# Performance work log

Hardware: AMD Instinct MI355X
Metric: run time of the kernel (lower is better)

Reference implementation:

```python
import jax, jax.numpy as jnp
import numpy as np

WS = 8          # window_size
H = 4           # num_heads
C = 128         # embed_dim
D = C // H      # head_dim
L = WS * WS     # tokens per window
B = 4096        # batch * num_windows


def _make_rel_index(ws):
    coords = np.stack(np.meshgrid(np.arange(ws), np.arange(ws), indexing='ij'))  # [2,ws,ws]
    flat = coords.reshape(2, -1)                       # [2, L]
    rel = flat[:, :, None] - flat[:, None, :]          # [2, L, L]
    rel = rel.transpose(1, 2, 0) + ws - 1              # [L, L, 2]
    return (rel[..., 0] * (2 * ws - 1) + rel[..., 1]).astype(np.int32)  # [L, L]


def setup_inputs() -> dict:
    key = jax.random.key(0)
    ks = jax.random.split(key, 10)
    s = 0.02
    return {
        'query': jax.random.normal(ks[0], (B, L, C), jnp.float32),
        'Wq': jax.random.normal(ks[1], (C, C), jnp.float32) * s,
        'bq': jnp.zeros((C,), jnp.float32),
        'Wk': jax.random.normal(ks[2], (C, C), jnp.float32) * s,
        'bk': jnp.zeros((C,), jnp.float32),
        'Wv': jax.random.normal(ks[3], (C, C), jnp.float32) * s,
        'bv': jnp.zeros((C,), jnp.float32),
        'Wo': jax.random.normal(ks[4], (C, C), jnp.float32) * s,
        'bo': jnp.zeros((C,), jnp.float32),
        'bias_table': jax.random.normal(ks[5], ((2 * WS - 1) ** 2, H), jnp.float32) * s,
        'rel_index': jnp.asarray(_make_rel_index(WS)),
    }


def reference(query, Wq, bq, Wk, bk, Wv, bv, Wo, bo, bias_table, rel_index):
    scale = D ** -0.5
    # projections (torch Linear: x @ W.T + b)
    q = (query @ Wq.T + bq).reshape(B, L, H, D).transpose(0, 2, 1, 3)  # [B,H,L,D]
    k = (query @ Wk.T + bk).reshape(B, L, H, D).transpose(0, 2, 1, 3)
    v = (query @ Wv.T + bv).reshape(B, L, H, D).transpose(0, 2, 1, 3)
    attn = jnp.einsum('bhqd,bhkd->bhqk', q, k) * scale               # [B,H,L,L]
    bias = bias_table[rel_index]                                      # [L,L,H]
    attn = attn + bias.transpose(2, 0, 1)[None]                       # add RPB
    attn = jax.nn.softmax(attn, axis=-1)
    out = jnp.einsum('bhqk,bhkd->bqhd', attn, v).reshape(B, L, C)
    out = out @ Wo.T + bo
    return out
```

## Files before the change

### kernel.cpp

```cpp
#include <hip/hip_runtime.h>
#include <hip/hip_bf16.h>

typedef unsigned int u32;
typedef unsigned short u16;
typedef __attribute__((ext_vector_type(8))) short short8;
typedef __attribute__((ext_vector_type(4))) float f32x4;
typedef __attribute__((ext_vector_type(2))) u32 u32x2;

#define LOG2E 1.4426950408889634f
#define SCALE 0.17677669529663687f

__device__ __forceinline__ u16 f2bf(float f) {
    return __builtin_bit_cast(u16, __float2bfloat16(f));
}
__device__ __forceinline__ u32 pkbf(float a, float b) {
    return (u32)f2bf(a) | ((u32)f2bf(b) << 16);
}

__device__ __forceinline__ int sw128(int r, int e) { return r * 128 + (e ^ ((r & 7) << 3)); }
__device__ __forceinline__ int sw64 (int r, int e) { return r * 64  + (e ^ ((r & 7) << 3)); }

__global__ __launch_bounds__(256) void prep_kernel(
    const float* __restrict__ Wq, const float* __restrict__ Wk,
    const float* __restrict__ Wv, const float* __restrict__ Wo,
    const float* __restrict__ bias_table, const int* __restrict__ rel_index,
    u16* __restrict__ wsW, float* __restrict__ wsB)
{
    int idx = blockIdx.x * 256 + threadIdx.x;
    if (idx < 16384) {
        wsW[idx]         = f2bf(Wq[idx] * (SCALE * LOG2E));
        wsW[16384 + idx] = f2bf(Wk[idx]);
        wsW[32768 + idx] = f2bf(Wv[idx]);
        wsW[49152 + idx] = f2bf(Wo[idx]);
        int h = idx >> 12, t = (idx >> 8) & 15, l = (idx >> 2) & 63, r = idx & 3;
        int mt = t >> 2, nt = t & 3, g = l >> 4, c = l & 15;
        int kk = 16 * mt + 4 * g + r, q = 16 * nt + c;
        wsB[idx] = bias_table[rel_index[q * 64 + kk] * 4 + h] * LOG2E;
    }
}

__global__ __launch_bounds__(256, 3) void wattn_kernel(
    const float* __restrict__ x,
    const float* __restrict__ bq, const float* __restrict__ bk,
    const float* __restrict__ bv, const float* __restrict__ bo,
    const u16* __restrict__ Wbf, const float* __restrict__ biasT,
    float* __restrict__ out)
{
    __shared__ u16 smem[24576];

    const int b    = blockIdx.x;
    const int tid  = threadIdx.x;
    const int wid  = tid >> 6;
    const int lane = tid & 63;
    const int g    = lane >> 4;
    const int c    = lane & 15;

    u16* qk = smem + wid * 6144;
    u16* vT = qk + 4096;

    {
        const float* xb = x + (size_t)b * 8192;
        #pragma unroll
        for (int it = 0; it < 8; ++it) {
            int idx = it * 1024 + tid * 4;
            float4 v = *(const float4*)(xb + idx);
            int row = idx >> 7, col = idx & 127;
            u32x2 wv;
            wv.x = pkbf(v.x, v.y);
            wv.y = pkbf(v.z, v.w);
            *(u32x2*)&smem[sw128(row, col)] = wv;
        }
    }
    __syncthreads();

    short8 xa[4][4];
    #pragma unroll
    for (int mt = 0; mt < 4; ++mt)
        #pragma unroll
        for (int kt = 0; kt < 4; ++kt)
            xa[mt][kt] = *(const short8*)&smem[sw128(16 * mt + c, 32 * kt + 8 * g)];
    __syncthreads();

    const int h = wid, d0 = 32 * h;
    #pragma unroll
    for (int p = 0; p < 3; ++p) {
        const float* bp = (p == 0) ? bq : (p == 1) ? bk : bv;
        #pragma unroll
        for (int j = 0; j < 2; ++j) {
            int nt = 2 * h + j;
            float bcol = bp[16 * nt + c];
            if (p == 0) bcol *= (SCALE * LOG2E);
            f32x4 acc[4];
            #pragma unroll
            for (int mt = 0; mt < 4; ++mt) { f32x4 t = {bcol, bcol, bcol, bcol}; acc[mt] = t; }
            const u16* W = Wbf + p * 16384 + (16 * nt + c) * 128;
            #pragma unroll
            for (int kt = 0; kt < 4; ++kt) {
                short8 bfr = *(const short8*)(W + 32 * kt + 8 * g);
                #pragma unroll
                for (int mt = 0; mt < 4; ++mt)
                    acc[mt] = __builtin_amdgcn_mfma_f32_16x16x32_bf16(xa[mt][kt], bfr, acc[mt], 0, 0, 0);
            }
            if (p < 2) {
                int colb = p * 32 + 16 * j + c;
                #pragma unroll
                for (int mt = 0; mt < 4; ++mt)
                    #pragma unroll
                    for (int r = 0; r < 4; ++r)
                        qk[sw64(16 * mt + 4 * g + r, colb)] = f2bf(acc[mt][r]);
            } else {
                #pragma unroll
                for (int mt = 0; mt < 4; ++mt) {
                    u32x2 wv;
                    wv.x = pkbf(acc[mt][0], acc[mt][1]);
                    wv.y = pkbf(acc[mt][2], acc[mt][3]);
                    *(u32x2*)&vT[sw64(16 * j + c, 16 * mt + 4 * g)] = wv;
                }
            }
        }
    }

    short8 ka[4], qb[4];
    #pragma unroll
    for (int t = 0; t < 4; ++t) {
        qb[t] = *(const short8*)&qk[sw64(16 * t + c, 8 * g)];
        ka[t] = *(const short8*)&qk[sw64(16 * t + c, 32 + 8 * g)];
    }
    f32x4 accP[4][4];
    const f32x4* bT = (const f32x4*)(biasT + h * 4096);
    #pragma unroll
    for (int mt = 0; mt < 4; ++mt)
        #pragma unroll
        for (int nt = 0; nt < 4; ++nt)
            accP[mt][nt] = __builtin_amdgcn_mfma_f32_16x16x32_bf16(
                ka[mt], qb[nt], bT[(mt * 4 + nt) * 64 + lane], 0, 0, 0);

    float rinv[4];
    #pragma unroll
    for (int nt = 0; nt < 4; ++nt) {
        float m = accP[0][nt][0];
        #pragma unroll
        for (int mt = 0; mt < 4; ++mt)
            #pragma unroll
            for (int r = 0; r < 4; ++r) m = fmaxf(m, accP[mt][nt][r]);
        m = fmaxf(m, __shfl_xor(m, 16, 64));
        m = fmaxf(m, __shfl_xor(m, 32, 64));
        float s = 0.f;
        #pragma unroll
        for (int mt = 0; mt < 4; ++mt)
            #pragma unroll
            for (int r = 0; r < 4; ++r) {
                float e = exp2f(accP[mt][nt][r] - m);
                accP[mt][nt][r] = e;
                s += e;
            }
        s += __shfl_xor(s, 16, 64);
        s += __shfl_xor(s, 32, 64);
        rinv[nt] = 1.0f / s;
    }

    #pragma unroll
    for (int mt = 0; mt < 4; ++mt)
        #pragma unroll
        for (int nt = 0; nt < 4; ++nt) {
            u32x2 wv;
            wv.x = pkbf(accP[mt][nt][0], accP[mt][nt][1]);
            wv.y = pkbf(accP[mt][nt][2], accP[mt][nt][3]);
            *(u32x2*)&qk[sw64(16 * nt + c, 16 * mt + 4 * g)] = wv;
        }

    f32x4 accO[2][4];
    #pragma unroll
    for (int mD = 0; mD < 2; ++mD)
        #pragma unroll
        for (int nt = 0; nt < 4; ++nt) { f32x4 z = {0.f, 0.f, 0.f, 0.f}; accO[mD][nt] = z; }
    #pragma unroll
    for (int kt = 0; kt < 2; ++kt) {
        short8 va[2];
        #pragma unroll
        for (int mD = 0; mD < 2; ++mD)
            va[mD] = *(const short8*)&vT[sw64(16 * mD + c, 32 * kt + 8 * g)];
        #pragma unroll
        for (int nt = 0; nt < 4; ++nt) {
            short8 pb = *(const short8*)&qk[sw64(16 * nt + c, 32 * kt + 8 * g)];
            #pragma unroll
            for (int mD = 0; mD < 2; ++mD)
                accO[mD][nt] = __builtin_amdgcn_mfma_f32_16x16x32_bf16(va[mD], pb, accO[mD][nt], 0, 0, 0);
        }
    }
    __syncthreads();

    #pragma unroll
    for (int mD = 0; mD < 2; ++mD)
        #pragma unroll
        for (int nt = 0; nt < 4; ++nt) {
            float riv = rinv[nt];
            u32x2 wv;
            wv.x = pkbf(accO[mD][nt][0] * riv, accO[mD][nt][1] * riv);
            wv.y = pkbf(accO[mD][nt][2] * riv, accO[mD][nt][3] * riv);
            *(u32x2*)&smem[sw128(16 * nt + c, d0 + 16 * mD + 4 * g)] = wv;
        }
    __syncthreads();

    short8 ha[4][4];
    #pragma unroll
    for (int mt = 0; mt < 4; ++mt)
        #pragma unroll
        for (int kt = 0; kt < 4; ++kt)
            ha[mt][kt] = *(const short8*)&smem[sw128(16 * mt + c, 32 * kt + 8 * g)];
    const u16* Wo_ = Wbf + 3 * 16384;
    float* ob = out + (size_t)b * 8192;
    #pragma unroll
    for (int j = 0; j < 2; ++j) {
        int nt = 2 * wid + j;
        float bocol = bo[16 * nt + c];
        f32x4 acc[4];
        #pragma unroll
        for (int mt = 0; mt < 4; ++mt) { f32x4 t = {bocol, bocol, bocol, bocol}; acc[mt] = t; }
        const u16* W = Wo_ + (16 * nt + c) * 128;
        #pragma unroll
        for (int kt = 0; kt < 4; ++kt) {
            short8 wf = *(const short8*)(W + 32 * kt + 8 * g);
            #pragma unroll
            for (int mt = 0; mt < 4; ++mt)
                acc[mt] = __builtin_amdgcn_mfma_f32_16x16x32_bf16(ha[mt][kt], wf, acc[mt], 0, 0, 0);
        }
        #pragma unroll
        for (int mt = 0; mt < 4; ++mt)
            #pragma unroll
            for (int r = 0; r < 4; ++r)
                ob[(16 * mt + 4 * g + r) * 128 + 16 * nt + c] = acc[mt][r];
    }
}

extern "C" void kernel_launch(void* const* d_in, const int* in_sizes, int n_in,
                              void* d_out, int out_size, void* d_ws, size_t ws_size,
                              hipStream_t stream)
{
    const float* query      = (const float*)d_in[0];
    const float* Wq         = (const float*)d_in[1];
    const float* bq         = (const float*)d_in[2];
    const float* Wk         = (const float*)d_in[3];
    const float* bk         = (const float*)d_in[4];
    const float* Wv         = (const float*)d_in[5];
    const float* bv         = (const float*)d_in[6];
    const float* Wo         = (const float*)d_in[7];
    const float* bo         = (const float*)d_in[8];
    const float* bias_table = (const float*)d_in[9];
    const int*   rel_index  = (const int*)d_in[10];

    u16*   wsW = (u16*)d_ws;
    float* wsB = (float*)((char*)d_ws + 131072);

    prep_kernel<<<dim3(64), dim3(256), 0, stream>>>(Wq, Wk, Wv, Wo, bias_table, rel_index, wsW, wsB);
    wattn_kernel<<<dim3(4096), dim3(256), 0, stream>>>(query, bq, bk, bv, bo, wsW, wsB, (float*)d_out);
}
```

Measured before the change: 127.7 us.

## Keep Q/K/P in registers via transposed MFMA layouts and raise occupancy

The Q and K projections are computed in transposed orientation (W as the A operand) so their accumulator fragments can be packed directly into 16x16x16 bf16 MFMA operands for QK^T. This removes the per-wave LDS staging for Q, K and the softmax probabilities, which also feeds P·V from registers. Shared memory shrinks from 48KB to 32KB, launch bounds rise to 4 blocks per CU, and the output projection is transposed so each lane writes a float4. The risks are extra register pressure from holding packed fragments under a tighter occupancy target, and the smaller K=16 MFMA instructions.

```diff
diff --git a/kernel.cpp b/kernel.cpp
--- a/kernel.cpp
+++ b/kernel.cpp
@@ -3,7 +3,8 @@
 
 typedef unsigned int u32;
 typedef unsigned short u16;
-typedef __attribute__((ext_vector_type(8))) short short8;
+typedef __attribute__((ext_vector_type(8))) short bf16x8;
+typedef __attribute__((ext_vector_type(4))) short bf16x4;
 typedef __attribute__((ext_vector_type(4))) float f32x4;
 typedef __attribute__((ext_vector_type(2))) u32 u32x2;
 
@@ -16,6 +17,21 @@
 __device__ __forceinline__ u32 pkbf(float a, float b) {
     return (u32)f2bf(a) | ((u32)f2bf(b) << 16);
 }
+__device__ __forceinline__ bf16x4 pk4(f32x4 v) {
+    u32x2 p; p.x = pkbf(v[0], v[1]); p.y = pkbf(v[2], v[3]);
+    return __builtin_bit_cast(bf16x4, p);
+}
+
+#if __has_builtin(__builtin_amdgcn_mfma_f32_16x16x16bf16_1k)
+#define MFMA16(A, B, C) __builtin_amdgcn_mfma_f32_16x16x16bf16_1k((A), (B), (C), 0, 0, 0)
+#else
+__device__ __forceinline__ f32x4 mfma16_fb(bf16x4 a, bf16x4 b, f32x4 c) {
+    bf16x8 a8 = {a[0], a[1], a[2], a[3], 0, 0, 0, 0};
+    bf16x8 b8 = {b[0], b[1], b[2], b[3], 0, 0, 0, 0};
+    return __builtin_amdgcn_mfma_f32_16x16x32_bf16(a8, b8, c, 0, 0, 0);
+}
+#define MFMA16(A, B, C) mfma16_fb((A), (B), (C))
+#endif
 
 __device__ __forceinline__ int sw128(int r, int e) { return r * 128 + (e ^ ((r & 7) << 3)); }
 __device__ __forceinline__ int sw64 (int r, int e) { return r * 64  + (e ^ ((r & 7) << 3)); }
@@ -39,14 +55,47 @@
     }
 }
 
-__global__ __launch_bounds__(256, 3) void wattn_kernel(
+__device__ __forceinline__ void proj_qk(
+    const u16* __restrict__ Xs, const u16* __restrict__ W,
+    const float* __restrict__ bp, float bscale,
+    int h, int g, int c, bf16x4 opk[4][2])
+{
+    f32x4 acc[2][4];
+    #pragma unroll
+    for (int CT = 0; CT < 2; ++CT) {
+        float4 bb = *(const float4*)&bp[32 * h + 16 * CT + 4 * g];
+        f32x4 bi = {bb.x * bscale, bb.y * bscale, bb.z * bscale, bb.w * bscale};
+        #pragma unroll
+        for (int nt = 0; nt < 4; ++nt) acc[CT][nt] = bi;
+    }
+    #pragma unroll
+    for (int kt = 0; kt < 4; ++kt) {
+        bf16x8 xs[4];
+        #pragma unroll
+        for (int nt = 0; nt < 4; ++nt)
+            xs[nt] = *(const bf16x8*)&Xs[sw128(16 * nt + c, 32 * kt + 8 * g)];
+        #pragma unroll
+        for (int CT = 0; CT < 2; ++CT) {
+            bf16x8 wf = *(const bf16x8*)(W + (32 * h + 16 * CT + c) * 128 + 32 * kt + 8 * g);
+            #pragma unroll
+            for (int nt = 0; nt < 4; ++nt)
+                acc[CT][nt] = __builtin_amdgcn_mfma_f32_16x16x32_bf16(wf, xs[nt], acc[CT][nt], 0, 0, 0);
+        }
+    }
+    #pragma unroll
+    for (int nt = 0; nt < 4; ++nt)
+        #pragma unroll
+        for (int CT = 0; CT < 2; ++CT) opk[nt][CT] = pk4(acc[CT][nt]);
+}
+
+__global__ __launch_bounds__(256, 4) void wattn_kernel(
     const float* __restrict__ x,
     const float* __restrict__ bq, const float* __restrict__ bk,
     const float* __restrict__ bv, const float* __restrict__ bo,
     const u16* __restrict__ Wbf, const float* __restrict__ biasT,
     float* __restrict__ out)
 {
-    __shared__ u16 smem[24576];
+    __shared__ u16 smem[16384];
 
     const int b    = blockIdx.x;
     const int tid  = threadIdx.x;
@@ -54,9 +103,10 @@
     const int lane = tid & 63;
     const int g    = lane >> 4;
     const int c    = lane & 15;
-
-    u16* qk = smem + wid * 6144;
-    u16* vT = qk + 4096;
+    const int h    = wid;
+
+    u16* Xs = smem;
+    u16* vT = smem + 8192 + wid * 2048;
 
     {
         const float* xb = x + (size_t)b * 8192;
@@ -68,81 +118,74 @@
             u32x2 wv;
             wv.x = pkbf(v.x, v.y);
             wv.y = pkbf(v.z, v.w);
-            *(u32x2*)&smem[sw128(row, col)] = wv;
+            *(u32x2*)&Xs[sw128(row, col)] = wv;
         }
     }
     __syncthreads();
 
-    short8 xa[4][4];
-    #pragma unroll
-    for (int mt = 0; mt < 4; ++mt)
-        #pragma unroll
-        for (int kt = 0; kt < 4; ++kt)
-            xa[mt][kt] = *(const short8*)&smem[sw128(16 * mt + c, 32 * kt + 8 * g)];
-    __syncthreads();
-
-    const int h = wid, d0 = 32 * h;
-    #pragma unroll
-    for (int p = 0; p < 3; ++p) {
-        const float* bp = (p == 0) ? bq : (p == 1) ? bk : bv;
+    bf16x4 qpk[4][2], kpk[4][2];
+    proj_qk(Xs, Wbf,         bq, SCALE * LOG2E, h, g, c, qpk);
+    proj_qk(Xs, Wbf + 16384, bk, 1.0f,          h, g, c, kpk);
+
+    {
+        const u16* Wv_ = Wbf + 32768;
+        f32x4 acc[2][4];
         #pragma unroll
         for (int j = 0; j < 2; ++j) {
-            int nt = 2 * h + j;
-            float bcol = bp[16 * nt + c];
-            if (p == 0) bcol *= (SCALE * LOG2E);
-            f32x4 acc[4];
-            #pragma unroll
-            for (int mt = 0; mt < 4; ++mt) { f32x4 t = {bcol, bcol, bcol, bcol}; acc[mt] = t; }
-            const u16* W = Wbf + p * 16384 + (16 * nt + c) * 128;
-            #pragma unroll
-            for (int kt = 0; kt < 4; ++kt) {
-                short8 bfr = *(const short8*)(W + 32 * kt + 8 * g);
+            float bcol = bv[32 * h + 16 * j + c];
+            #pragma unroll
+            for (int mt = 0; mt < 4; ++mt) { f32x4 t = {bcol, bcol, bcol, bcol}; acc[j][mt] = t; }
+        }
+        #pragma unroll
+        for (int kt = 0; kt < 4; ++kt) {
+            bf16x8 xs[4];
+            #pragma unroll
+            for (int mt = 0; mt < 4; ++mt)
+                xs[mt] = *(const bf16x8*)&Xs[sw128(16 * mt + c, 32 * kt + 8 * g)];
+            #pragma unroll
+            for (int j = 0; j < 2; ++j) {
+                bf16x8 wf = *(const bf16x8*)(Wv_ + (32 * h + 16 * j + c) * 128 + 32 * kt + 8 * g);
                 #pragma unroll
                 for (int mt = 0; mt < 4; ++mt)
-                    acc[mt] = __builtin_amdgcn_mfma_f32_16x16x32_bf16(xa[mt][kt], bfr, acc[mt], 0, 0, 0);
-            }
-            if (p < 2) {
-                int colb = p * 32 + 16 * j + c;
-                #pragma unroll
-                for (int mt = 0; mt < 4; ++mt)
-                    #pragma unroll
-                    for (int r = 0; r < 4; ++r)
-                        qk[sw64(16 * mt + 4 * g + r, colb)] = f2bf(acc[mt][r]);
-            } else {
-                #pragma unroll
-                for (int mt = 0; mt < 4; ++mt) {
-                    u32x2 wv;
-                    wv.x = pkbf(acc[mt][0], acc[mt][1]);
-                    wv.y = pkbf(acc[mt][2], acc[mt][3]);
-                    *(u32x2*)&vT[sw64(16 * j + c, 16 * mt + 4 * g)] = wv;
-                }
-            }
-        }
-    }
-
-    short8 ka[4], qb[4];
-    #pragma unroll
-    for (int t = 0; t < 4; ++t) {
-        qb[t] = *(const short8*)&qk[sw64(16 * t + c, 8 * g)];
-        ka[t] = *(const short8*)&qk[sw64(16 * t + c, 32 + 8 * g)];
-    }
-    f32x4 accP[4][4];
-    const f32x4* bT = (const f32x4*)(biasT + h * 4096);
-    #pragma unroll
-    for (int mt = 0; mt < 4; ++mt)
-        #pragma unroll
-        for (int nt = 0; nt < 4; ++nt)
-            accP[mt][nt] = __builtin_amdgcn_mfma_f32_16x16x32_bf16(
-                ka[mt], qb[nt], bT[(mt * 4 + nt) * 64 + lane], 0, 0, 0);
+                    acc[j][mt] = __builtin_amdgcn_mfma_f32_16x16x32_bf16(xs[mt], wf, acc[j][mt], 0, 0, 0);
+            }
+        }
+        #pragma unroll
+        for (int j = 0; j < 2; ++j)
+            #pragma unroll
+            for (int mt = 0; mt < 4; ++mt) {
+                u32x2 wv;
+                wv.x = pkbf(acc[j][mt][0], acc[j][mt][1]);
+                wv.y = pkbf(acc[j][mt][2], acc[j][mt][3]);
+                *(u32x2*)&vT[sw64(16 * j + c, 16 * mt + 4 * g)] = wv;
+            }
+    }
+
+    f32x4 accS[4][4];
+    {
+        const f32x4* bT = (const f32x4*)(biasT + h * 4096);
+        #pragma unroll
+        for (int mt = 0; mt < 4; ++mt)
+            #pragma unroll
+            for (int nt = 0; nt < 4; ++nt)
+                accS[mt][nt] = bT[(mt * 4 + nt) * 64 + lane];
+        #pragma unroll
+        for (int mt = 0; mt < 4; ++mt)
+            #pragma unroll
+            for (int nt = 0; nt < 4; ++nt) {
+                accS[mt][nt] = MFMA16(kpk[mt][0], qpk[nt][0], accS[mt][nt]);
+                accS[mt][nt] = MFMA16(kpk[mt][1], qpk[nt][1], accS[mt][nt]);
+            }
+    }
 
     float rinv[4];
     #pragma unroll
     for (int nt = 0; nt < 4; ++nt) {
-        float m = accP[0][nt][0];
-        #pragma unroll
-        for (int mt = 0; mt < 4; ++mt)
-            #pragma unroll
-            for (int r = 0; r < 4; ++r) m = fmaxf(m, accP[mt][nt][r]);
+        float m = accS[0][nt][0];
+        #pragma unroll
+        for (int mt = 0; mt < 4; ++mt)
+            #pragma unroll
+            for (int r = 0; r < 4; ++r) m = fmaxf(m, accS[mt][nt][r]);
         m = fmaxf(m, __shfl_xor(m, 16, 64));
         m = fmaxf(m, __shfl_xor(m, 32, 64));
         float s = 0.f;
@@ -150,8 +193,8 @@
         for (int mt = 0; mt < 4; ++mt)
             #pragma unroll
             for (int r = 0; r < 4; ++r) {
-                float e = exp2f(accP[mt][nt][r] - m);
-                accP[mt][nt][r] = e;
+                float e = exp2f(accS[mt][nt][r] - m);
+                accS[mt][nt][r] = e;
                 s += e;
             }
         s += __shfl_xor(s, 16, 64);
@@ -159,15 +202,11 @@
         rinv[nt] = 1.0f / s;
     }
 
+    bf16x4 ppk[4][4];
     #pragma unroll
     for (int mt = 0; mt < 4; ++mt)
         #pragma unroll
-        for (int nt = 0; nt < 4; ++nt) {
-            u32x2 wv;
-            wv.x = pkbf(accP[mt][nt][0], accP[mt][nt][1]);
-            wv.y = pkbf(accP[mt][nt][2], accP[mt][nt][3]);
-            *(u32x2*)&qk[sw64(16 * nt + c, 16 * mt + 4 * g)] = wv;
-        }
+        for (int nt = 0; nt < 4; ++nt) ppk[mt][nt] = pk4(accS[mt][nt]);
 
     f32x4 accO[2][4];
     #pragma unroll
@@ -175,18 +214,16 @@
         #pragma unroll
         for (int nt = 0; nt < 4; ++nt) { f32x4 z = {0.f, 0.f, 0.f, 0.f}; accO[mD][nt] = z; }
     #pragma unroll
-    for (int kt = 0; kt < 2; ++kt) {
-        short8 va[2];
-        #pragma unroll
-        for (int mD = 0; mD < 2; ++mD)
-            va[mD] = *(const short8*)&vT[sw64(16 * mD + c, 32 * kt + 8 * g)];
-        #pragma unroll
-        for (int nt = 0; nt < 4; ++nt) {
-            short8 pb = *(const short8*)&qk[sw64(16 * nt + c, 32 * kt + 8 * g)];
-            #pragma unroll
-            for (int mD = 0; mD < 2; ++mD)
-                accO[mD][nt] = __builtin_amdgcn_mfma_f32_16x16x32_bf16(va[mD], pb, accO[mD][nt], 0, 0, 0);
-        }
+    for (int mD = 0; mD < 2; ++mD) {
+        bf16x4 vf[4];
+        #pragma unroll
+        for (int mt = 0; mt < 4; ++mt)
+            vf[mt] = *(const bf16x4*)&vT[sw64(16 * mD + c, 16 * mt + 4 * g)];
+        #pragma unroll
+        for (int nt = 0; nt < 4; ++nt)
+            #pragma unroll
+            for (int mt = 0; mt < 4; ++mt)
+                accO[mD][nt] = MFMA16(vf[mt], ppk[mt][nt], accO[mD][nt]);
     }
     __syncthreads();
 
@@ -198,38 +235,35 @@
             u32x2 wv;
             wv.x = pkbf(accO[mD][nt][0] * riv, accO[mD][nt][1] * riv);
             wv.y = pkbf(accO[mD][nt][2] * riv, accO[mD][nt][3] * riv);
-            *(u32x2*)&smem[sw128(16 * nt + c, d0 + 16 * mD + 4 * g)] = wv;
+            *(u32x2*)&Xs[sw128(16 * nt + c, 32 * h + 16 * mD + 4 * g)] = wv;
         }
     __syncthreads();
 
-    short8 ha[4][4];
-    #pragma unroll
-    for (int mt = 0; mt < 4; ++mt)
+    bf16x8 ha[4][4];
+    #pragma unroll
+    for (int nt = 0; nt < 4; ++nt)
         #pragma unroll
         for (int kt = 0; kt < 4; ++kt)
-            ha[mt][kt] = *(const short8*)&smem[sw128(16 * mt + c, 32 * kt + 8 * g)];
-    const u16* Wo_ = Wbf + 3 * 16384;
+            ha[nt][kt] = *(const bf16x8*)&Xs[sw128(16 * nt + c, 32 * kt + 8 * g)];
+    const u16* Wo_ = Wbf + 49152;
     float* ob = out + (size_t)b * 8192;
     #pragma unroll
     for (int j = 0; j < 2; ++j) {
-        int nt = 2 * wid + j;
-        float bocol = bo[16 * nt + c];
+        int OT = 2 * wid + j;
+        float4 bb = *(const float4*)&bo[16 * OT + 4 * g];
         f32x4 acc[4];
         #pragma unroll
-        for (int mt = 0; mt < 4; ++mt) { f32x4 t = {bocol, bocol, bocol, bocol}; acc[mt] = t; }
-        const u16* W = Wo_ + (16 * nt + c) * 128;
+        for (int nt = 0; nt < 4; ++nt) { f32x4 t = {bb.x, bb.y, bb.z, bb.w}; acc[nt] = t; }
         #pragma unroll
         for (int kt = 0; kt < 4; ++kt) {
-            short8 wf = *(const short8*)(W + 32 * kt + 8 * g);
-            #pragma unroll
-            for (int mt = 0; mt < 4; ++mt)
-                acc[mt] = __builtin_amdgcn_mfma_f32_16x16x32_bf16(ha[mt][kt], wf, acc[mt], 0, 0, 0);
-        }
-        #pragma unroll
-        for (int mt = 0; mt < 4; ++mt)
-            #pragma unroll
-            for (int r = 0; r < 4; ++r)
-                ob[(16 * mt + 4 * g + r) * 128 + 16 * nt + c] = acc[mt][r];
+            bf16x8 wof = *(const bf16x8*)(Wo_ + (16 * OT + c) * 128 + 32 * kt + 8 * g);
+            #pragma unroll
+            for (int nt = 0; nt < 4; ++nt)
+                acc[nt] = __builtin_amdgcn_mfma_f32_16x16x32_bf16(wof, ha[nt][kt], acc[nt], 0, 0, 0);
+        }
+        #pragma unroll
+        for (int nt = 0; nt < 4; ++nt)
+            *(f32x4*)&ob[(16 * nt + c) * 128 + 16 * OT + 4 * g] = acc[nt];
     }
 }
 
```

Result: slower. 167.5 us (+31.1%).
